# Kernel optimization log

Hardware: AMD Instinct MI355X
Metric: run time of the kernel (lower is better)

Reference implementation:

```python
import jax, jax.numpy as jnp
import numpy as np

B, N, P, E = 64, 512, 256, 4096          # batch, nodes (stations), partition nodes, edges
NUM_NWP, LP, F = 8, 16, 32               # num_nwp, local_points, local_cnn_dims
NT, ED, H, W = 8, 8, 64, 8               # num_temp, edge_feature_dims, decf_mlp_hidden, weight_function_dim
G, RH = 64, 256                          # gnn_dim, readout_hid_dim
H1, Q = 128, 9                           # mlp_hid_dim1, num quantiles


def setup_inputs() -> dict:
    key = jax.random.key(0)
    ks = iter(jax.random.split(key, 40))
    def rn(shape, s=0.05):
        return jax.random.normal(next(ks), shape, dtype=jnp.float32) * s
    # one-hot incidence matrices: each edge has one left (partition) node and one right node
    lidx = jax.random.randint(next(ks), (E,), 0, P)
    ridx = jax.random.randint(next(ks), (E,), 0, N)
    linc = jnp.zeros((P, E), jnp.float32).at[lidx, jnp.arange(E)].set(1.0)
    rinc = jnp.zeros((E, N), jnp.float32).at[jnp.arange(E), ridx].set(1.0)
    inp = {
        "x1": jax.random.normal(next(ks), (B, NUM_NWP * N, LP), dtype=jnp.float32),
        "x2": jax.random.normal(next(ks), (B, NT), dtype=jnp.float32),
        # LocalConv1D grouped conv (torch OIW layout: [Cout, Cin/groups, K])
        "conv_w": rn((F * N, NUM_NWP, LP)), "conv_b": rn((F * N,)),
        # WDSGCN2 edge-weight MLP
        "k1_w": rn((H, ED)), "k1_b": rn((H,)),
        "k2_w": rn((H, NT)),
        "k3_w": rn((H, F)),
        "k4_w": rn((H, F)),
        "k5_w": rn((W, H)), "k5_b": rn((W,)),
        "gc_w": rn((G, F * W)), "gc_b": rn((G,)),
        # readout
        "r0_w": rn((RH, G * P)),
        "r1_w": rn((RH, NT)), "r1_b": rn((RH,)),
        "r2_w": rn((RH, P)),
        "r3_w": rn((P, RH)), "r3_b": rn((P,)),
        # SMlp (forward uses l1 -> ELU -> l3 only)
        "l1_w": rn((H1, NT + G)), "l1_b": rn((H1,)),
        "l3_w": rn((Q, H1)), "l3_b": rn((Q,)),
        # buffers
        "ef": jax.random.normal(next(ks), (E, ED + 1), dtype=jnp.float32),
        "linc": linc,
        "rinc": rinc,
        "cap_feature": jax.random.normal(next(ks), (P,), dtype=jnp.float32),
        "partition_idx": jnp.arange(P, dtype=jnp.int32) * (N // P),
    }
    return inp


def reference(x1, x2, conv_w, conv_b, k1_w, k1_b, k2_w, k3_w, k4_w, k5_w, k5_b,
              gc_w, gc_b, r0_w, r1_w, r1_b, r2_w, r3_w, r3_b,
              l1_w, l1_b, l3_w, l3_b, ef, linc, rinc, cap_feature, partition_idx):
    b = x1.shape[0]
    # --- LocalConv1D: grouped conv1d (valid padding, output length 1) + ReLU ---
    y = jax.lax.conv_general_dilated(x1, conv_w, (1,), 'VALID',
                                     dimension_numbers=('NCH', 'OIH', 'NCH'),
                                     feature_group_count=N)
    x = jax.nn.relu(y + conv_b[None, :, None]).reshape(b, N, F)      # [B,N,F]
    # --- WDSGCN2: per-edge weight kernel ---
    kern = ef[:, :-1] @ k1_w.T + k1_b                                # [E,H]
    kern = kern[None] + (x2 @ k2_w.T)[:, None, :]                    # [B,E,H]
    xp = x[:, partition_idx, :]                                      # [B,P,F]
    kern = kern + jnp.einsum('pe,bpf->bef', linc, xp) @ k3_w.T       # left-node feats
    rx = jnp.einsum('en,bnf->bef', rinc, x)                          # right-node feats [B,E,F]
    kern = kern + rx @ k4_w.T
    kern = jax.nn.relu(jax.nn.leaky_relu(kern, 0.02) @ k5_w.T + k5_b)  # [B,E,W]
    # --- message = kernel (outer) right-node features, aggregated by left incidence ---
    msg = kern[:, :, :, None] * rx[:, :, None, :]                    # [B,E,W,F]
    agg = jnp.einsum('pe,bewf->bpwf', linc, msg).reshape(b, P, W * F)
    yg = jax.nn.relu(agg @ gc_w.T + gc_b)                            # [B,P,G]
    # --- readout attention over partition nodes ---
    h = yg.reshape(b, -1) @ r0_w.T + (x2 @ r1_w.T + r1_b) + cap_feature @ r2_w.T
    wt = jax.nn.relu(jax.nn.leaky_relu(h, 0.01) @ r3_w.T + r3_b)     # [B,P]
    res = jnp.einsum('bp,bpg->bg', wt, yg)                           # [B,G]
    # --- SMlp head ---
    z = jnp.concatenate([res, x2], axis=1)
    z = jax.nn.elu(z @ l1_w.T + l1_b)
    return z @ l3_w.T + l3_b                                         # [B,Q]
```

## Files before the change

kernel.cpp:

```cpp
#include <hip/hip_runtime.h>
#include <math.h>

#define B_ 64
#define N_ 512
#define P_ 256
#define E_ 4096
#define F_ 32
#define H_ 64
#define W_ 8
#define G_ 64
#define RH_ 256

#define X_OFF   0
#define T4_OFF  (X_OFF + N_*B_*F_)
#define T3_OFF  (T4_OFF + N_*B_*H_)
#define KB_OFF  (T3_OFF + P_*B_*H_)
#define KW_OFF  (KB_OFF + E_*H_)
#define YG_OFF  (KW_OFF + E_*B_*W_)
#define HB_OFF  (YG_OFF + B_*P_*G_)
#define RES_OFF (HB_OFF + B_*RH_)
#define INT_OFF (RES_OFF + 4*B_*G_)

__global__ __launch_bounds__(256) void k_decode(const float* __restrict__ linc,
    const float* __restrict__ rinc, int* __restrict__ lidx, int* __restrict__ ridx) {
  int i4 = blockIdx.x * 256 + threadIdx.x;
  const int L4 = (P_ * E_) / 4;
  if (i4 < L4) {
    float4 v = ((const float4*)linc)[i4];
    int i = i4 * 4;
    int p = i >> 12, e = i & 4095;
    if (v.x != 0.0f) lidx[e]     = p;
    if (v.y != 0.0f) lidx[e + 1] = p;
    if (v.z != 0.0f) lidx[e + 2] = p;
    if (v.w != 0.0f) lidx[e + 3] = p;
  } else {
    int j4 = i4 - L4;
    float4 v = ((const float4*)rinc)[j4];
    int j = j4 * 4;
    int e = j >> 9, n = j & 511;
    if (v.x != 0.0f) ridx[e] = n;
    if (v.y != 0.0f) ridx[e] = n + 1;
    if (v.z != 0.0f) ridx[e] = n + 2;
    if (v.w != 0.0f) ridx[e] = n + 3;
  }
}

__global__ __launch_bounds__(1024) void k_lists(const int* __restrict__ lidx,
    int* __restrict__ part_start, int* __restrict__ part_edges) {
  __shared__ int cnt[256];
  __shared__ int buf[256];
  __shared__ int cur[256];
  int t = threadIdx.x;
  if (t < 256) cnt[t] = 0;
  __syncthreads();
  for (int e = t; e < E_; e += 1024) atomicAdd(&cnt[lidx[e]], 1);
  __syncthreads();
  if (t < 256) buf[t] = cnt[t];
  __syncthreads();
  for (int off = 1; off < 256; off <<= 1) {
    int add = 0;
    if (t < 256 && t >= off) add = buf[t - off];
    __syncthreads();
    if (t < 256) buf[t] += add;
    __syncthreads();
  }
  if (t < 256) {
    part_start[t + 1] = buf[t];
    if (t == 0) part_start[0] = 0;
    cur[t] = buf[t] - cnt[t];
  }
  __syncthreads();
  for (int e = t; e < E_; e += 1024) {
    int p = lidx[e];
    int pos = atomicAdd(&cur[p], 1);
    part_edges[pos] = e;
  }
}

__global__ __launch_bounds__(256) void k_conv(const float* __restrict__ x1,
    const float* __restrict__ conv_w, const float* __restrict__ conv_b,
    float* __restrict__ x) {
  __shared__ float wsm[32 * 132];
  __shared__ float xsm[8192];
  int n = blockIdx.x, t = threadIdx.x;
  for (int i = t; i < 1024; i += 256) {
    int f = i >> 5, j = i & 31;
    ((float4*)wsm)[f * 33 + j] = ((const float4*)(conv_w + n * 4096))[i];
  }
  for (int i = t; i < 2048; i += 256) {
    int b = i >> 5, j = i & 31;
    ((float4*)xsm)[i] = ((const float4*)(x1 + b * 65536 + n * 128))[j];
  }
  __syncthreads();
  int f = t & 31, bq = t >> 5;
  float cb = conv_b[n * 32 + f];
  float acc[8];
#pragma unroll
  for (int bi = 0; bi < 8; bi++) acc[bi] = cb;
  const float4* wf4 = (const float4*)wsm + f * 33;
  const float4* xb4 = (const float4*)xsm + bq * 256;
#pragma unroll 4
  for (int k4 = 0; k4 < 32; k4++) {
    float4 wv = wf4[k4];
#pragma unroll
    for (int bi = 0; bi < 8; bi++) {
      float4 xv = xb4[bi * 32 + k4];
      acc[bi] += wv.x * xv.x + wv.y * xv.y + wv.z * xv.z + wv.w * xv.w;
    }
  }
#pragma unroll
  for (int bi = 0; bi < 8; bi++) {
    int b = bq * 8 + bi;
    x[n * 2048 + b * 32 + f] = fmaxf(acc[bi], 0.0f);
  }
}

__global__ __launch_bounds__(256) void k_prep(
    const float* __restrict__ x, const int* __restrict__ pidx,
    const float* __restrict__ k3_w, const float* __restrict__ k4_w,
    const float* __restrict__ x2, const float* __restrict__ k2_w,
    const float* __restrict__ ef, const float* __restrict__ k1_w,
    const float* __restrict__ k1_b,
    const float* __restrict__ r1_w, const float* __restrict__ r1_b,
    const float* __restrict__ r2_w, const float* __restrict__ cap,
    float* __restrict__ t4, float* __restrict__ t3, float* __restrict__ kb,
    float* __restrict__ hbuf) {
  __shared__ float xsh[2048];
  __shared__ float wsh[64 * 36];
  __shared__ float x2s[512];
  __shared__ float k2s[512];
  int blk = blockIdx.x, t = threadIdx.x;
  if (blk < 768) {
    bool isT4 = blk < 512;
    int n = isT4 ? blk : pidx[blk - 512];
    const float* wmat = isT4 ? k4_w : k3_w;
    float* outp = isT4 ? (t4 + blk * 4096) : (t3 + (blk - 512) * 4096);
    for (int i = t; i < 512; i += 256) {
      ((float4*)xsh)[i] = ((const float4*)(x + n * 2048))[i];
      int h = i >> 3, j = i & 7;
      ((float4*)wsh)[h * 9 + j] = ((const float4*)wmat)[i];
    }
    if (isT4) {
      for (int i = t; i < 128; i += 256) {
        ((float4*)x2s)[i] = ((const float4*)x2)[i];
        ((float4*)k2s)[i] = ((const float4*)k2_w)[i];
      }
    }
    __syncthreads();
    int h = t & 63, bq = t >> 6;
    float wreg[32];
#pragma unroll
    for (int j = 0; j < 8; j++) {
      float4 v = ((float4*)wsh)[h * 9 + j];
      wreg[4 * j] = v.x; wreg[4 * j + 1] = v.y; wreg[4 * j + 2] = v.z; wreg[4 * j + 3] = v.w;
    }
    float w2[8];
    if (isT4) {
      float4 u = ((float4*)k2s)[h * 2], v = ((float4*)k2s)[h * 2 + 1];
      w2[0] = u.x; w2[1] = u.y; w2[2] = u.z; w2[3] = u.w;
      w2[4] = v.x; w2[5] = v.y; w2[6] = v.z; w2[7] = v.w;
    }
    for (int bi = 0; bi < 16; bi++) {
      int b = bq * 16 + bi;
      float acc = 0.0f;
#pragma unroll
      for (int j = 0; j < 8; j++) {
        float4 xv = ((float4*)xsh)[b * 8 + j];
        acc += xv.x * wreg[4 * j] + xv.y * wreg[4 * j + 1] +
               xv.z * wreg[4 * j + 2] + xv.w * wreg[4 * j + 3];
      }
      if (isT4) {
        float4 u = ((float4*)x2s)[b * 2], v = ((float4*)x2s)[b * 2 + 1];
        acc += u.x * w2[0] + u.y * w2[1] + u.z * w2[2] + u.w * w2[3] +
               v.x * w2[4] + v.y * w2[5] + v.z * w2[6] + v.w * w2[7];
      }
      outp[b * 64 + h] = acc;
    }
  } else if (blk < 1792) {
    int o = (blk - 768) * 256 + t;
    int e = o >> 6, h = o & 63;
    float acc = k1_b[h];
    const float* er = ef + e * 9;
    const float* kr = k1_w + h * 8;
#pragma unroll
    for (int d = 0; d < 8; d++) acc += er[d] * kr[d];
    kb[o] = acc;
  } else {
    int o = (blk - 1792) * 256 + t;
    int rh = o & 255;
    float acc = r1_b[rh];
    const float* xr = x2 + (o >> 8) * 8;
    const float* rr = r1_w + rh * 8;
#pragma unroll
    for (int d = 0; d < 8; d++) acc += xr[d] * rr[d];
    const float* r2r = r2_w + rh * 256;
    for (int p4 = 0; p4 < 64; p4++) {
      float4 cv = ((const float4*)cap)[p4];
      float4 rv = ((const float4*)r2r)[p4];
      acc += cv.x * rv.x + cv.y * rv.y + cv.z * rv.z + cv.w * rv.w;
    }
    hbuf[o] = acc;
  }
}

__global__ __launch_bounds__(256) void k_eagg(
    const float* __restrict__ x, const float* __restrict__ kb,
    const float* __restrict__ t3, const float* __restrict__ t4,
    const float* __restrict__ k5_w, const float* __restrict__ k5_b,
    const int* __restrict__ ridx, const int* __restrict__ part_start,
    const int* __restrict__ part_edges,
    const float* __restrict__ gc_w, const float* __restrict__ gc_b,
    float* __restrict__ yg) {
  __shared__ float t3s[64 * 68];
  __shared__ float k5t[4 * 520];
  __shared__ unsigned short accS[64 * 256];
  int p = blockIdx.x, t = threadIdx.x;
  for (int i = t; i < 512; i += 256) {
    int h = i >> 3, w = i & 7;
    float v = k5_w[w * 64 + h];
#pragma unroll
    for (int qq = 0; qq < 4; qq++) k5t[qq * 520 + i] = v;
  }
  for (int i4 = t; i4 < 1024; i4 += 256) {
    float4 v = ((const float4*)(t3 + p * 4096))[i4];
    *(float4*)(t3s + (i4 >> 4) * 68 + (i4 & 15) * 4) = v;
  }
  __syncthreads();
  int s = t & 3, b = t >> 2;
  const float* kq = k5t + s * 520 + s * 128;
  float kb5_0 = k5_b[2 * s], kb5_1 = k5_b[2 * s + 1];
  const float4* t3p = (const float4*)(t3s + b * 68 + s * 16);
  float acc[64];
#pragma unroll
  for (int j = 0; j < 64; j++) acc[j] = 0.0f;
  int s0 = part_start[p], s1 = part_start[p + 1];
  int e = 0, r = 0;
  if (s0 < s1) { e = part_edges[s0]; r = ridx[e]; }
  for (int idx = s0; idx < s1; idx++) {
    int e_n = 0, r_n = 0;
    if (idx + 1 < s1) { e_n = part_edges[idx + 1]; r_n = ridx[e_n]; }
    const float4* xp = (const float4*)(x + r * 2048 + b * 32);
    float4 xv0 = xp[0], xv1 = xp[1], xv2 = xp[2], xv3 = xp[3];
    float4 xv4 = xp[4], xv5 = xp[5], xv6 = xp[6], xv7 = xp[7];
    const float4* kb4 = (const float4*)(kb + e * 64 + s * 16);
    const float4* t44 = (const float4*)(t4 + r * 4096 + b * 64 + s * 16);
    float lk[16];
#pragma unroll
    for (int j4 = 0; j4 < 4; j4++) {
      float4 a = kb4[j4], c = t3p[j4], d = t44[j4];
      float v;
      v = a.x + c.x + d.x; lk[j4 * 4 + 0] = v > 0.0f ? v : 0.02f * v;
      v = a.y + c.y + d.y; lk[j4 * 4 + 1] = v > 0.0f ? v : 0.02f * v;
      v = a.z + c.z + d.z; lk[j4 * 4 + 2] = v > 0.0f ? v : 0.02f * v;
      v = a.w + c.w + d.w; lk[j4 * 4 + 3] = v > 0.0f ? v : 0.02f * v;
    }
    float pw[8] = {0, 0, 0, 0, 0, 0, 0, 0};
#pragma unroll
    for (int j = 0; j < 16; j++) {
      float4 u = *(const float4*)(kq + j * 8);
      float4 v = *(const float4*)(kq + j * 8 + 4);
      float l = lk[j];
      pw[0] += l * u.x; pw[1] += l * u.y; pw[2] += l * u.z; pw[3] += l * u.w;
      pw[4] += l * v.x; pw[5] += l * v.y; pw[6] += l * v.z; pw[7] += l * v.w;
    }
#pragma unroll
    for (int w = 0; w < 8; w++) {
      pw[w] += __shfl_xor(pw[w], 1);
      pw[w] += __shfl_xor(pw[w], 2);
    }
    float kv0 = fmaxf(pw[2 * s] + kb5_0, 0.0f);
    float kv1 = fmaxf(pw[2 * s + 1] + kb5_1, 0.0f);
    float xa[32];
    xa[0] = xv0.x; xa[1] = xv0.y; xa[2] = xv0.z; xa[3] = xv0.w;
    xa[4] = xv1.x; xa[5] = xv1.y; xa[6] = xv1.z; xa[7] = xv1.w;
    xa[8] = xv2.x; xa[9] = xv2.y; xa[10] = xv2.z; xa[11] = xv2.w;
    xa[12] = xv3.x; xa[13] = xv3.y; xa[14] = xv3.z; xa[15] = xv3.w;
    xa[16] = xv4.x; xa[17] = xv4.y; xa[18] = xv4.z; xa[19] = xv4.w;
    xa[20] = xv5.x; xa[21] = xv5.y; xa[22] = xv5.z; xa[23] = xv5.w;
    xa[24] = xv6.x; xa[25] = xv6.y; xa[26] = xv6.z; xa[27] = xv6.w;
    xa[28] = xv7.x; xa[29] = xv7.y; xa[30] = xv7.z; xa[31] = xv7.w;
#pragma unroll
    for (int j = 0; j < 32; j++) acc[j] += kv0 * xa[j];
#pragma unroll
    for (int j = 0; j < 32; j++) acc[32 + j] += kv1 * xa[j];
    e = e_n; r = r_n;
  }
#pragma unroll
  for (int o = 0; o < 8; o++) {
    int koct = s * 8 + o;
    int os = koct ^ (b >> 3);
    unsigned int wds[4];
#pragma unroll
    for (int h = 0; h < 4; h++) {
      unsigned int u0 = __float_as_uint(acc[o * 8 + 2 * h]);
      u0 = u0 + 0x7fffu + ((u0 >> 16) & 1u);
      unsigned int u1 = __float_as_uint(acc[o * 8 + 2 * h + 1]);
      u1 = u1 + 0x7fffu + ((u1 >> 16) & 1u);
      wds[h] = (u0 >> 16) | (u1 & 0xffff0000u);
    }
    int4 pk = make_int4((int)wds[0], (int)wds[1], (int)wds[2], (int)wds[3]);
    *(int4*)(accS + b * 256 + os * 8) = pk;
  }
  __syncthreads();
  int lane = t & 63, wv = t >> 6;
  int bg = lane >> 3, gg = lane & 7;
  int g0 = wv * 16 + gg * 2;
  const float* gw0 = gc_w + g0 * 256;
  const float* gw1 = gc_w + (g0 + 1) * 256;
  float ac[8][2];
#pragma unroll
  for (int i = 0; i < 8; i++) { ac[i][0] = 0.0f; ac[i][1] = 0.0f; }
  for (int oct = 0; oct < 32; oct++) {
    int4 a8[8];
#pragma unroll
    for (int i = 0; i < 8; i++) {
      int row = bg * 8 + i;
      int os = oct ^ bg;
      a8[i] = *(const int4*)(accS + row * 256 + os * 8);
    }
    float4 b0a = *(const float4*)(gw0 + oct * 8);
    float4 b0b = *(const float4*)(gw0 + oct * 8 + 4);
    float4 b1a = *(const float4*)(gw1 + oct * 8);
    float4 b1b = *(const float4*)(gw1 + oct * 8 + 4);
    float bv0[8] = {b0a.x, b0a.y, b0a.z, b0a.w, b0b.x, b0b.y, b0b.z, b0b.w};
    float bv1[8] = {b1a.x, b1a.y, b1a.z, b1a.w, b1b.x, b1b.y, b1b.z, b1b.w};
#pragma unroll
    for (int kk = 0; kk < 8; kk++) {
#pragma unroll
      for (int i = 0; i < 8; i++) {
        int w32;
        switch (kk >> 1) {
          case 0: w32 = a8[i].x; break;
          case 1: w32 = a8[i].y; break;
          case 2: w32 = a8[i].z; break;
          default: w32 = a8[i].w; break;
        }
        unsigned int u = (unsigned int)w32;
        unsigned int bits = (kk & 1) ? (u & 0xffff0000u) : (u << 16);
        float av = __uint_as_float(bits);
        ac[i][0] += av * bv0[kk];
        ac[i][1] += av * bv1[kk];
      }
    }
  }
  float gb0 = gc_b[g0], gb1 = gc_b[g0 + 1];
#pragma unroll
  for (int i = 0; i < 8; i++) {
    int bb = bg * 8 + i;
    float* yp = yg + bb * 16384 + p * 64;
    yp[g0]     = fmaxf(ac[i][0] + gb0, 0.0f);
    yp[g0 + 1] = fmaxf(ac[i][1] + gb1, 0.0f);
  }
}

__global__ __launch_bounds__(256) void k_r0(const float* __restrict__ yg,
    const float* __restrict__ r0_w, float* __restrict__ part) {
  __shared__ float ygs[64 * 68];
  __shared__ float wts[64 * 260];
  int kc = blockIdx.x, t = threadIdx.x;
  int k0 = kc * 64;
  {
    int c = t >> 4, rr = t & 15;
    for (int rd = 0; rd < 16; rd++) {
      int rh = rd * 16 + rr;
      float4 v = *(const float4*)(r0_w + rh * 16384 + k0 + c * 4);
      wts[(4 * c + 0) * 260 + rh] = v.x;
      wts[(4 * c + 1) * 260 + rh] = v.y;
      wts[(4 * c + 2) * 260 + rh] = v.z;
      wts[(4 * c + 3) * 260 + rh] = v.w;
    }
  }
  {
    int b = t >> 2, kq = t & 3;
    const float* src = yg + b * 16384 + k0 + kq * 16;
#pragma unroll
    for (int u = 0; u < 4; u++) {
      float4 v = *(const float4*)(src + u * 4);
      int kk = kq * 16 + u * 4;
      ygs[(kk + 0) * 68 + b] = v.x;
      ygs[(kk + 1) * 68 + b] = v.y;
      ygs[(kk + 2) * 68 + b] = v.z;
      ygs[(kk + 3) * 68 + b] = v.w;
    }
  }
  __syncthreads();
  int lane = t & 63, wv = t >> 6;
  int b8 = lane & 7, r8 = lane >> 3;
  const float* yp = ygs + b8 * 8;
  const float* wp = wts + wv * 64 + r8 * 8;
  float acc[8][8];
#pragma unroll
  for (int i = 0; i < 8; i++)
#pragma unroll
    for (int j = 0; j < 8; j++) acc[i][j] = 0.0f;
#pragma unroll 2
  for (int k = 0; k < 64; k++) {
    float4 ya = *(const float4*)(yp + k * 68);
    float4 yb = *(const float4*)(yp + k * 68 + 4);
    float4 wa = *(const float4*)(wp + k * 260);
    float4 wb = *(const float4*)(wp + k * 260 + 4);
    float yv[8] = {ya.x, ya.y, ya.z, ya.w, yb.x, yb.y, yb.z, yb.w};
    float wr[8] = {wa.x, wa.y, wa.z, wa.w, wb.x, wb.y, wb.z, wb.w};
#pragma unroll
    for (int i = 0; i < 8; i++)
#pragma unroll
      for (int j = 0; j < 8; j++) acc[i][j] += yv[i] * wr[j];
  }
  float* pb = part + kc * 16384 + wv * 64 + r8 * 8;
#pragma unroll
  for (int i = 0; i < 8; i++) {
    float4 s0 = make_float4(acc[i][0], acc[i][1], acc[i][2], acc[i][3]);
    float4 s1 = make_float4(acc[i][4], acc[i][5], acc[i][6], acc[i][7]);
    float* pp = pb + (b8 * 8 + i) * 256;
    *(float4*)pp = s0;
    *(float4*)(pp + 4) = s1;
  }
}

__global__ __launch_bounds__(256) void k_r0red(const float* __restrict__ part,
    float* __restrict__ hbuf) {
  int blk = blockIdx.x;
  int oq = blk & 63, kq = blk >> 6;
  int o = oq * 256 + threadIdx.x;
  float s = 0.0f;
  const float* pp = part + kq * 64 * 16384 + o;
#pragma unroll 8
  for (int kc = 0; kc < 64; kc++) s += pp[kc * 16384];
  atomicAdd(&hbuf[o], s);
}

__global__ __launch_bounds__(256) void k_wt_res(const float* __restrict__ hbuf,
    const float* __restrict__ r3_w, const float* __restrict__ r3_b,
    const float* __restrict__ yg, float* __restrict__ res4) {
  __shared__ float hs[256];
  __shared__ float wts[64];
  __shared__ float red[256];
  int blk = blockIdx.x;
  int bb = blk >> 2, pq = blk & 3;
  int t = threadIdx.x;
  float hv = hbuf[bb * 256 + t];
  hs[t] = hv > 0.0f ? hv : 0.01f * hv;
  __syncthreads();
  int pl = t >> 2, c = t & 3;
  int pp = pq * 64 + pl;
  const float4* wrow = (const float4*)(r3_w + pp * 256 + c * 64);
  const float4* h4 = (const float4*)(hs) + c * 16;
  float a = 0.0f;
#pragma unroll
  for (int j = 0; j < 16; j++) {
    float4 w4 = wrow[j], hh = h4[j];
    a += hh.x * w4.x + hh.y * w4.y + hh.z * w4.z + hh.w * w4.w;
  }
  a += __shfl_xor(a, 1);
  a += __shfl_xor(a, 2);
  if (c == 0) wts[pl] = fmaxf(a + r3_b[pp], 0.0f);
  __syncthreads();
  int g = t & 63, ch = t >> 6;
  float r = 0.0f;
  const float* ygp = yg + bb * 16384 + pq * 4096 + g;
#pragma unroll
  for (int pi = 0; pi < 16; pi++) {
    int pl2 = ch * 16 + pi;
    r += wts[pl2] * ygp[pl2 * 64];
  }
  red[t] = r;
  __syncthreads();
  if (t < 64)
    res4[pq * 4096 + bb * 64 + t] = red[t] + red[t + 64] + red[t + 128] + red[t + 192];
}

__global__ __launch_bounds__(128) void k_final(const float* __restrict__ res4,
    const float* __restrict__ x2, const float* __restrict__ l1_w,
    const float* __restrict__ l1_b, const float* __restrict__ l3_w,
    const float* __restrict__ l3_b, float* __restrict__ out) {
  __shared__ float zs[128];
  int bb = blockIdx.x, t = threadIdx.x;
  float acc = l1_b[t];
  const float* wrow = l1_w + t * 72;
  const float* rr = res4 + bb * 64;
#pragma unroll 8
  for (int j = 0; j < 64; j++) {
    float rv = rr[j] + rr[4096 + j] + rr[8192 + j] + rr[12288 + j];
    acc += rv * wrow[j];
  }
  const float* xr = x2 + bb * 8;
#pragma unroll
  for (int j = 0; j < 8; j++) acc += xr[j] * wrow[64 + j];
  zs[t] = acc > 0.0f ? acc : expm1f(acc);
  __syncthreads();
  if (t < 9) {
    float o = l3_b[t];
    const float* w3 = l3_w + t * 128;
    for (int j = 0; j < 128; j++) o += zs[j] * w3[j];
    out[bb * 9 + t] = o;
  }
}

extern "C" void kernel_launch(void* const* d_in, const int* in_sizes, int n_in,
                              void* d_out, int out_size, void* d_ws, size_t ws_size,
                              hipStream_t stream) {
  (void)in_sizes; (void)n_in; (void)out_size; (void)ws_size;
  const float* x1     = (const float*)d_in[0];
  const float* x2     = (const float*)d_in[1];
  const float* conv_w = (const float*)d_in[2];
  const float* conv_b = (const float*)d_in[3];
  const float* k1_w   = (const float*)d_in[4];
  const float* k1_b   = (const float*)d_in[5];
  const float* k2_w   = (const float*)d_in[6];
  const float* k3_w   = (const float*)d_in[7];
  const float* k4_w   = (const float*)d_in[8];
  const float* k5_w   = (const float*)d_in[9];
  const float* k5_b   = (const float*)d_in[10];
  const float* gc_w   = (const float*)d_in[11];
  const float* gc_b   = (const float*)d_in[12];
  const float* r0_w   = (const float*)d_in[13];
  const float* r1_w   = (const float*)d_in[14];
  const float* r1_b   = (const float*)d_in[15];
  const float* r2_w   = (const float*)d_in[16];
  const float* r3_w   = (const float*)d_in[17];
  const float* r3_b   = (const float*)d_in[18];
  const float* l1_w   = (const float*)d_in[19];
  const float* l1_b   = (const float*)d_in[20];
  const float* l3_w   = (const float*)d_in[21];
  const float* l3_b   = (const float*)d_in[22];
  const float* ef     = (const float*)d_in[23];
  const float* linc   = (const float*)d_in[24];
  const float* rinc   = (const float*)d_in[25];
  const float* cap    = (const float*)d_in[26];
  const int*   pidx   = (const int*)d_in[27];
  float* out = (float*)d_out;

  float* ws   = (float*)d_ws;
  float* xbuf = ws + X_OFF;
  float* t4   = ws + T4_OFF;
  float* t3   = ws + T3_OFF;
  float* kb   = ws + KB_OFF;
  float* yg   = ws + YG_OFF;
  float* hbuf = ws + HB_OFF;
  float* res4 = ws + RES_OFF;
  float* part = ws + X_OFF;
  int* ib = (int*)(ws + INT_OFF);
  int* lidx = ib;
  int* ridx = ib + 4096;
  int* part_start = ib + 8192;
  int* part_edges = ib + 8704;

  hipLaunchKernelGGL(k_decode, dim3(3072), dim3(256), 0, stream, linc, rinc, lidx, ridx);
  hipLaunchKernelGGL(k_lists, dim3(1), dim3(1024), 0, stream, lidx, part_start, part_edges);
  hipLaunchKernelGGL(k_conv, dim3(512), dim3(256), 0, stream, x1, conv_w, conv_b, xbuf);
  hipLaunchKernelGGL(k_prep, dim3(1856), dim3(256), 0, stream,
                     xbuf, pidx, k3_w, k4_w, x2, k2_w, ef, k1_w, k1_b,
                     r1_w, r1_b, r2_w, cap, t4, t3, kb, hbuf);
  hipLaunchKernelGGL(k_eagg, dim3(256), dim3(256), 0, stream,
                     xbuf, kb, t3, t4, k5_w, k5_b, ridx, part_start, part_edges,
                     gc_w, gc_b, yg);
  hipLaunchKernelGGL(k_r0, dim3(256), dim3(256), 0, stream, yg, r0_w, part);
  hipLaunchKernelGGL(k_r0red, dim3(256), dim3(256), 0, stream, part, hbuf);
  hipLaunchKernelGGL(k_wt_res, dim3(256), dim3(256), 0, stream, hbuf, r3_w, r3_b, yg, res4);
  hipLaunchKernelGGL(k_final, dim3(64), dim3(128), 0, stream,
                     res4, x2, l1_w, l1_b, l3_w, l3_b, out);
}
```

Baseline: 260.5 us.

## Split edge-aggregation kernel across batch quarters with 16 threads per batch row

The edge-aggregation kernel now launches four blocks per partition node, each handling 16 batch rows, with 16 threads cooperating per batch row instead of 4. Each thread keeps only 16 accumulators instead of 64 and holds the k5 weights in registers rather than shared memory. An extra shuffle reduction across the hidden dimension is added. The gc_w projection is remapped so each thread computes 4 outputs for one row and writes them as a float4. The aim is to lower register pressure, raise occupancy and give the GPU more blocks to spread across its compute units, at the cost of more shuffles and gc_w reads repeated across four blocks.

Result: slower. 331.8 us (+27.4%).

```diff
diff --git a/kernel.cpp b/kernel.cpp
--- a/kernel.cpp
+++ b/kernel.cpp
@@ -203,7 +203,7 @@
   }
 }
 
-__global__ __launch_bounds__(256) void k_eagg(
+__global__ __launch_bounds__(256, 4) void k_eagg(
     const float* __restrict__ x, const float* __restrict__ kb,
     const float* __restrict__ t3, const float* __restrict__ t4,
     const float* __restrict__ k5_w, const float* __restrict__ k5_b,
@@ -211,146 +211,136 @@
     const int* __restrict__ part_edges,
     const float* __restrict__ gc_w, const float* __restrict__ gc_b,
     float* __restrict__ yg) {
-  __shared__ float t3s[64 * 68];
-  __shared__ float k5t[4 * 520];
-  __shared__ unsigned short accS[64 * 256];
-  int p = blockIdx.x, t = threadIdx.x;
-  for (int i = t; i < 512; i += 256) {
-    int h = i >> 3, w = i & 7;
-    float v = k5_w[w * 64 + h];
-#pragma unroll
-    for (int qq = 0; qq < 4; qq++) k5t[qq * 520 + i] = v;
-  }
-  for (int i4 = t; i4 < 1024; i4 += 256) {
-    float4 v = ((const float4*)(t3 + p * 4096))[i4];
-    *(float4*)(t3s + (i4 >> 4) * 68 + (i4 & 15) * 4) = v;
-  }
-  __syncthreads();
-  int s = t & 3, b = t >> 2;
-  const float* kq = k5t + s * 520 + s * 128;
-  float kb5_0 = k5_b[2 * s], kb5_1 = k5_b[2 * s + 1];
-  const float4* t3p = (const float4*)(t3s + b * 68 + s * 16);
-  float acc[64];
-#pragma unroll
-  for (int j = 0; j < 64; j++) acc[j] = 0.0f;
+  __shared__ unsigned short accS[16 * 256];
+  int blk = blockIdx.x;
+  int p = blk >> 2, bh = blk & 3;
+  int t = threadIdx.x;
+  int s = t & 15, bl = t >> 4;
+  int bg = bh * 16 + bl;
+  int j = s & 3;
+  int q = s >> 2;
+  int f0 = q * 8;
+  float4 kr4[8];
+#pragma unroll
+  for (int w = 0; w < 8; w++)
+    kr4[w] = *(const float4*)(k5_w + w * 64 + s * 4);
+  float kb5_0 = k5_b[2 * j], kb5_1 = k5_b[2 * j + 1];
+  float4 t3r = *(const float4*)(t3 + p * 4096 + bg * 64 + s * 4);
+  float acc0[8], acc1[8];
+#pragma unroll
+  for (int i = 0; i < 8; i++) { acc0[i] = 0.0f; acc1[i] = 0.0f; }
   int s0 = part_start[p], s1 = part_start[p + 1];
   int e = 0, r = 0;
   if (s0 < s1) { e = part_edges[s0]; r = ridx[e]; }
   for (int idx = s0; idx < s1; idx++) {
     int e_n = 0, r_n = 0;
     if (idx + 1 < s1) { e_n = part_edges[idx + 1]; r_n = ridx[e_n]; }
-    const float4* xp = (const float4*)(x + r * 2048 + b * 32);
-    float4 xv0 = xp[0], xv1 = xp[1], xv2 = xp[2], xv3 = xp[3];
-    float4 xv4 = xp[4], xv5 = xp[5], xv6 = xp[6], xv7 = xp[7];
-    const float4* kb4 = (const float4*)(kb + e * 64 + s * 16);
-    const float4* t44 = (const float4*)(t4 + r * 4096 + b * 64 + s * 16);
-    float lk[16];
-#pragma unroll
-    for (int j4 = 0; j4 < 4; j4++) {
-      float4 a = kb4[j4], c = t3p[j4], d = t44[j4];
-      float v;
-      v = a.x + c.x + d.x; lk[j4 * 4 + 0] = v > 0.0f ? v : 0.02f * v;
-      v = a.y + c.y + d.y; lk[j4 * 4 + 1] = v > 0.0f ? v : 0.02f * v;
-      v = a.z + c.z + d.z; lk[j4 * 4 + 2] = v > 0.0f ? v : 0.02f * v;
-      v = a.w + c.w + d.w; lk[j4 * 4 + 3] = v > 0.0f ? v : 0.02f * v;
-    }
-    float pw[8] = {0, 0, 0, 0, 0, 0, 0, 0};
-#pragma unroll
-    for (int j = 0; j < 16; j++) {
-      float4 u = *(const float4*)(kq + j * 8);
-      float4 v = *(const float4*)(kq + j * 8 + 4);
-      float l = lk[j];
-      pw[0] += l * u.x; pw[1] += l * u.y; pw[2] += l * u.z; pw[3] += l * u.w;
-      pw[4] += l * v.x; pw[5] += l * v.y; pw[6] += l * v.z; pw[7] += l * v.w;
-    }
+    const float4* xp = (const float4*)(x + r * 2048 + bg * 32 + f0);
+    float4 xv0 = xp[0], xv1 = xp[1];
+    float4 a = *(const float4*)(kb + e * 64 + s * 4);
+    float4 d = *(const float4*)(t4 + r * 4096 + bg * 64 + s * 4);
+    float v, lk0, lk1, lk2, lk3;
+    v = a.x + t3r.x + d.x; lk0 = v > 0.0f ? v : 0.02f * v;
+    v = a.y + t3r.y + d.y; lk1 = v > 0.0f ? v : 0.02f * v;
+    v = a.z + t3r.z + d.z; lk2 = v > 0.0f ? v : 0.02f * v;
+    v = a.w + t3r.w + d.w; lk3 = v > 0.0f ? v : 0.02f * v;
+    float pw[8];
+#pragma unroll
+    for (int w = 0; w < 8; w++)
+      pw[w] = lk0 * kr4[w].x + lk1 * kr4[w].y + lk2 * kr4[w].z + lk3 * kr4[w].w;
 #pragma unroll
     for (int w = 0; w < 8; w++) {
       pw[w] += __shfl_xor(pw[w], 1);
       pw[w] += __shfl_xor(pw[w], 2);
     }
-    float kv0 = fmaxf(pw[2 * s] + kb5_0, 0.0f);
-    float kv1 = fmaxf(pw[2 * s + 1] + kb5_1, 0.0f);
-    float xa[32];
-    xa[0] = xv0.x; xa[1] = xv0.y; xa[2] = xv0.z; xa[3] = xv0.w;
-    xa[4] = xv1.x; xa[5] = xv1.y; xa[6] = xv1.z; xa[7] = xv1.w;
-    xa[8] = xv2.x; xa[9] = xv2.y; xa[10] = xv2.z; xa[11] = xv2.w;
-    xa[12] = xv3.x; xa[13] = xv3.y; xa[14] = xv3.z; xa[15] = xv3.w;
-    xa[16] = xv4.x; xa[17] = xv4.y; xa[18] = xv4.z; xa[19] = xv4.w;
-    xa[20] = xv5.x; xa[21] = xv5.y; xa[22] = xv5.z; xa[23] = xv5.w;
-    xa[24] = xv6.x; xa[25] = xv6.y; xa[26] = xv6.z; xa[27] = xv6.w;
-    xa[28] = xv7.x; xa[29] = xv7.y; xa[30] = xv7.z; xa[31] = xv7.w;
-#pragma unroll
-    for (int j = 0; j < 32; j++) acc[j] += kv0 * xa[j];
-#pragma unroll
-    for (int j = 0; j < 32; j++) acc[32 + j] += kv1 * xa[j];
+    float pa = j == 0 ? pw[0] : j == 1 ? pw[2] : j == 2 ? pw[4] : pw[6];
+    float pb = j == 0 ? pw[1] : j == 1 ? pw[3] : j == 2 ? pw[5] : pw[7];
+    pa += __shfl_xor(pa, 4); pa += __shfl_xor(pa, 8);
+    pb += __shfl_xor(pb, 4); pb += __shfl_xor(pb, 8);
+    float kv0 = fmaxf(pa + kb5_0, 0.0f);
+    float kv1 = fmaxf(pb + kb5_1, 0.0f);
+    float xa[8] = {xv0.x, xv0.y, xv0.z, xv0.w, xv1.x, xv1.y, xv1.z, xv1.w};
+#pragma unroll
+    for (int i = 0; i < 8; i++) acc0[i] += kv0 * xa[i];
+#pragma unroll
+    for (int i = 0; i < 8; i++) acc1[i] += kv1 * xa[i];
     e = e_n; r = r_n;
   }
-#pragma unroll
-  for (int o = 0; o < 8; o++) {
-    int koct = s * 8 + o;
-    int os = koct ^ (b >> 3);
+  {
     unsigned int wds[4];
 #pragma unroll
     for (int h = 0; h < 4; h++) {
-      unsigned int u0 = __float_as_uint(acc[o * 8 + 2 * h]);
+      unsigned int u0 = __float_as_uint(acc0[2 * h]);
       u0 = u0 + 0x7fffu + ((u0 >> 16) & 1u);
-      unsigned int u1 = __float_as_uint(acc[o * 8 + 2 * h + 1]);
+      unsigned int u1 = __float_as_uint(acc0[2 * h + 1]);
       u1 = u1 + 0x7fffu + ((u1 >> 16) & 1u);
       wds[h] = (u0 >> 16) | (u1 & 0xffff0000u);
     }
-    int4 pk = make_int4((int)wds[0], (int)wds[1], (int)wds[2], (int)wds[3]);
-    *(int4*)(accS + b * 256 + os * 8) = pk;
+    int oct = 8 * j + q;
+    int os = oct ^ (bl & 7);
+    *(int4*)(accS + bl * 256 + os * 8) =
+        make_int4((int)wds[0], (int)wds[1], (int)wds[2], (int)wds[3]);
+#pragma unroll
+    for (int h = 0; h < 4; h++) {
+      unsigned int u0 = __float_as_uint(acc1[2 * h]);
+      u0 = u0 + 0x7fffu + ((u0 >> 16) & 1u);
+      unsigned int u1 = __float_as_uint(acc1[2 * h + 1]);
+      u1 = u1 + 0x7fffu + ((u1 >> 16) & 1u);
+      wds[h] = (u0 >> 16) | (u1 & 0xffff0000u);
+    }
+    oct = 8 * j + 4 + q;
+    os = oct ^ (bl & 7);
+    *(int4*)(accS + bl * 256 + os * 8) =
+        make_int4((int)wds[0], (int)wds[1], (int)wds[2], (int)wds[3]);
   }
   __syncthreads();
   int lane = t & 63, wv = t >> 6;
-  int bg = lane >> 3, gg = lane & 7;
-  int g0 = wv * 16 + gg * 2;
+  int row = lane >> 2;
+  int gg = lane & 3;
+  int g0 = wv * 16 + gg * 4;
   const float* gw0 = gc_w + g0 * 256;
-  const float* gw1 = gc_w + (g0 + 1) * 256;
-  float ac[8][2];
-#pragma unroll
-  for (int i = 0; i < 8; i++) { ac[i][0] = 0.0f; ac[i][1] = 0.0f; }
+  const float* gw1 = gw0 + 256;
+  const float* gw2 = gw0 + 512;
+  const float* gw3 = gw0 + 768;
+  float ac0 = 0.0f, ac1 = 0.0f, ac2 = 0.0f, ac3 = 0.0f;
   for (int oct = 0; oct < 32; oct++) {
-    int4 a8[8];
-#pragma unroll
-    for (int i = 0; i < 8; i++) {
-      int row = bg * 8 + i;
-      int os = oct ^ bg;
-      a8[i] = *(const int4*)(accS + row * 256 + os * 8);
-    }
+    int os = oct ^ (row & 7);
+    int4 a8 = *(const int4*)(accS + row * 256 + os * 8);
     float4 b0a = *(const float4*)(gw0 + oct * 8);
     float4 b0b = *(const float4*)(gw0 + oct * 8 + 4);
     float4 b1a = *(const float4*)(gw1 + oct * 8);
     float4 b1b = *(const float4*)(gw1 + oct * 8 + 4);
+    float4 b2a = *(const float4*)(gw2 + oct * 8);
+    float4 b2b = *(const float4*)(gw2 + oct * 8 + 4);
+    float4 b3a = *(const float4*)(gw3 + oct * 8);
+    float4 b3b = *(const float4*)(gw3 + oct * 8 + 4);
     float bv0[8] = {b0a.x, b0a.y, b0a.z, b0a.w, b0b.x, b0b.y, b0b.z, b0b.w};
     float bv1[8] = {b1a.x, b1a.y, b1a.z, b1a.w, b1b.x, b1b.y, b1b.z, b1b.w};
+    float bv2[8] = {b2a.x, b2a.y, b2a.z, b2a.w, b2b.x, b2b.y, b2b.z, b2b.w};
+    float bv3[8] = {b3a.x, b3a.y, b3a.z, b3a.w, b3b.x, b3b.y, b3b.z, b3b.w};
 #pragma unroll
     for (int kk = 0; kk < 8; kk++) {
-#pragma unroll
-      for (int i = 0; i < 8; i++) {
-        int w32;
-        switch (kk >> 1) {
-          case 0: w32 = a8[i].x; break;
-          case 1: w32 = a8[i].y; break;
-          case 2: w32 = a8[i].z; break;
-          default: w32 = a8[i].w; break;
-        }
-        unsigned int u = (unsigned int)w32;
-        unsigned int bits = (kk & 1) ? (u & 0xffff0000u) : (u << 16);
-        float av = __uint_as_float(bits);
-        ac[i][0] += av * bv0[kk];
-        ac[i][1] += av * bv1[kk];
+      int w32;
+      switch (kk >> 1) {
+        case 0: w32 = a8.x; break;
+        case 1: w32 = a8.y; break;
+        case 2: w32 = a8.z; break;
+        default: w32 = a8.w; break;
       }
-    }
-  }
-  float gb0 = gc_b[g0], gb1 = gc_b[g0 + 1];
-#pragma unroll
-  for (int i = 0; i < 8; i++) {
-    int bb = bg * 8 + i;
-    float* yp = yg + bb * 16384 + p * 64;
-    yp[g0]     = fmaxf(ac[i][0] + gb0, 0.0f);
-    yp[g0 + 1] = fmaxf(ac[i][1] + gb1, 0.0f);
-  }
+      unsigned int u = (unsigned int)w32;
+      unsigned int bits = (kk & 1) ? (u & 0xffff0000u) : (u << 16);
+      float av = __uint_as_float(bits);
+      ac0 += av * bv0[kk];
+      ac1 += av * bv1[kk];
+      ac2 += av * bv2[kk];
+      ac3 += av * bv3[kk];
+    }
+  }
+  float4 gb = *(const float4*)(gc_b + g0);
+  float* yp = yg + (bh * 16 + row) * 16384 + p * 64 + g0;
+  float4 o = make_float4(fmaxf(ac0 + gb.x, 0.0f), fmaxf(ac1 + gb.y, 0.0f),
+                         fmaxf(ac2 + gb.z, 0.0f), fmaxf(ac3 + gb.w, 0.0f));
+  *(float4*)yp = o;
 }
 
 __global__ __launch_bounds__(256) void k_r0(const float* __restrict__ yg,
@@ -551,7 +541,7 @@
   hipLaunchKernelGGL(k_prep, dim3(1856), dim3(256), 0, stream,
                      xbuf, pidx, k3_w, k4_w, x2, k2_w, ef, k1_w, k1_b,
                      r1_w, r1_b, r2_w, cap, t4, t3, kb, hbuf);
-  hipLaunchKernelGGL(k_eagg, dim3(256), dim3(256), 0, stream,
+  hipLaunchKernelGGL(k_eagg, dim3(1024), dim3(256), 0, stream,
                      xbuf, kb, t3, t4, k5_w, k5_b, ridx, part_start, part_edges,
                      gc_w, gc_b, yg);
   hipLaunchKernelGGL(k_r0, dim3(256), dim3(256), 0, stream, yg, r0_w, part);
```

## Merge setup kernels, split edge loop across two slots, drop bf16 staging

Applied to the files above, without the earlier changes.

The incidence decode and conv kernels are merged into one launch. The edge-list build moves into an extra block of the prep kernel and stores (edge, right-node) pairs together. The edge aggregation kernel now uses 512 threads, with two slots each handling alternate edges of a partition. The slots reduce their partial sums through fp32 shared memory in two halves, and the gc projection reads gc_w directly, replacing the bf16-packed staging. The aim is fewer launches, more parallelism in the latency-bound edge loop, and no bf16 rounding, at the cost of extra syncs and higher register pressure from 512 threads each holding 64 accumulators.

New measurement: 258.7 us. No clear change (-0.7%).

```diff
diff --git a/kernel.cpp b/kernel.cpp
--- a/kernel.cpp
+++ b/kernel.cpp
@@ -21,68 +21,38 @@
 #define RES_OFF (HB_OFF + B_*RH_)
 #define INT_OFF (RES_OFF + 4*B_*G_)
 
-__global__ __launch_bounds__(256) void k_decode(const float* __restrict__ linc,
-    const float* __restrict__ rinc, int* __restrict__ lidx, int* __restrict__ ridx) {
-  int i4 = blockIdx.x * 256 + threadIdx.x;
-  const int L4 = (P_ * E_) / 4;
-  if (i4 < L4) {
-    float4 v = ((const float4*)linc)[i4];
-    int i = i4 * 4;
-    int p = i >> 12, e = i & 4095;
-    if (v.x != 0.0f) lidx[e]     = p;
-    if (v.y != 0.0f) lidx[e + 1] = p;
-    if (v.z != 0.0f) lidx[e + 2] = p;
-    if (v.w != 0.0f) lidx[e + 3] = p;
-  } else {
-    int j4 = i4 - L4;
-    float4 v = ((const float4*)rinc)[j4];
-    int j = j4 * 4;
-    int e = j >> 9, n = j & 511;
-    if (v.x != 0.0f) ridx[e] = n;
-    if (v.y != 0.0f) ridx[e] = n + 1;
-    if (v.z != 0.0f) ridx[e] = n + 2;
-    if (v.w != 0.0f) ridx[e] = n + 3;
-  }
-}
-
-__global__ __launch_bounds__(1024) void k_lists(const int* __restrict__ lidx,
-    int* __restrict__ part_start, int* __restrict__ part_edges) {
-  __shared__ int cnt[256];
-  __shared__ int buf[256];
-  __shared__ int cur[256];
-  int t = threadIdx.x;
-  if (t < 256) cnt[t] = 0;
-  __syncthreads();
-  for (int e = t; e < E_; e += 1024) atomicAdd(&cnt[lidx[e]], 1);
-  __syncthreads();
-  if (t < 256) buf[t] = cnt[t];
-  __syncthreads();
-  for (int off = 1; off < 256; off <<= 1) {
-    int add = 0;
-    if (t < 256 && t >= off) add = buf[t - off];
-    __syncthreads();
-    if (t < 256) buf[t] += add;
-    __syncthreads();
-  }
-  if (t < 256) {
-    part_start[t + 1] = buf[t];
-    if (t == 0) part_start[0] = 0;
-    cur[t] = buf[t] - cnt[t];
-  }
-  __syncthreads();
-  for (int e = t; e < E_; e += 1024) {
-    int p = lidx[e];
-    int pos = atomicAdd(&cur[p], 1);
-    part_edges[pos] = e;
-  }
-}
-
-__global__ __launch_bounds__(256) void k_conv(const float* __restrict__ x1,
-    const float* __restrict__ conv_w, const float* __restrict__ conv_b,
-    float* __restrict__ x) {
+__global__ __launch_bounds__(256) void k_dc(
+    const float* __restrict__ linc, const float* __restrict__ rinc,
+    int* __restrict__ lidx, int* __restrict__ ridx,
+    const float* __restrict__ x1, const float* __restrict__ conv_w,
+    const float* __restrict__ conv_b, float* __restrict__ x) {
   __shared__ float wsm[32 * 132];
   __shared__ float xsm[8192];
-  int n = blockIdx.x, t = threadIdx.x;
+  int blk = blockIdx.x, t = threadIdx.x;
+  if (blk < 3072) {
+    int i4 = blk * 256 + t;
+    const int L4 = (P_ * E_) / 4;
+    if (i4 < L4) {
+      float4 v = ((const float4*)linc)[i4];
+      int i = i4 * 4;
+      int p = i >> 12, e = i & 4095;
+      if (v.x != 0.0f) lidx[e]     = p;
+      if (v.y != 0.0f) lidx[e + 1] = p;
+      if (v.z != 0.0f) lidx[e + 2] = p;
+      if (v.w != 0.0f) lidx[e + 3] = p;
+    } else {
+      int j4 = i4 - L4;
+      float4 v = ((const float4*)rinc)[j4];
+      int j = j4 * 4;
+      int e = j >> 9, n = j & 511;
+      if (v.x != 0.0f) ridx[e] = n;
+      if (v.y != 0.0f) ridx[e] = n + 1;
+      if (v.z != 0.0f) ridx[e] = n + 2;
+      if (v.w != 0.0f) ridx[e] = n + 3;
+    }
+    return;
+  }
+  int n = blk - 3072;
   for (int i = t; i < 1024; i += 256) {
     int f = i >> 5, j = i & 31;
     ((float4*)wsm)[f * 33 + j] = ((const float4*)(conv_w + n * 4096))[i];
@@ -123,12 +93,17 @@
     const float* __restrict__ k1_b,
     const float* __restrict__ r1_w, const float* __restrict__ r1_b,
     const float* __restrict__ r2_w, const float* __restrict__ cap,
+    const int* __restrict__ lidx, const int* __restrict__ ridx,
     float* __restrict__ t4, float* __restrict__ t3, float* __restrict__ kb,
-    float* __restrict__ hbuf) {
+    float* __restrict__ hbuf, int* __restrict__ part_start,
+    int2* __restrict__ pe2) {
   __shared__ float xsh[2048];
   __shared__ float wsh[64 * 36];
   __shared__ float x2s[512];
   __shared__ float k2s[512];
+  __shared__ int cnt[256];
+  __shared__ int buf[256];
+  __shared__ int cur[256];
   int blk = blockIdx.x, t = threadIdx.x;
   if (blk < 768) {
     bool isT4 = blk < 512;
@@ -185,7 +160,7 @@
 #pragma unroll
     for (int d = 0; d < 8; d++) acc += er[d] * kr[d];
     kb[o] = acc;
-  } else {
+  } else if (blk < 1856) {
     int o = (blk - 1792) * 256 + t;
     int rh = o & 255;
     float acc = r1_b[rh];
@@ -200,33 +175,56 @@
       acc += cv.x * rv.x + cv.y * rv.y + cv.z * rv.z + cv.w * rv.w;
     }
     hbuf[o] = acc;
-  }
-}
-
-__global__ __launch_bounds__(256) void k_eagg(
+  } else {
+    cnt[t] = 0;
+    __syncthreads();
+    for (int e = t; e < E_; e += 256) atomicAdd(&cnt[lidx[e]], 1);
+    __syncthreads();
+    buf[t] = cnt[t];
+    __syncthreads();
+    for (int off = 1; off < 256; off <<= 1) {
+      int add = (t >= off) ? buf[t - off] : 0;
+      __syncthreads();
+      buf[t] += add;
+      __syncthreads();
+    }
+    part_start[t + 1] = buf[t];
+    if (t == 0) part_start[0] = 0;
+    cur[t] = buf[t] - cnt[t];
+    __syncthreads();
+    for (int e = t; e < E_; e += 256) {
+      int p = lidx[e];
+      int pos = atomicAdd(&cur[p], 1);
+      pe2[pos] = make_int2(e, ridx[e]);
+    }
+  }
+}
+
+__global__ __launch_bounds__(512) void k_eagg(
     const float* __restrict__ x, const float* __restrict__ kb,
     const float* __restrict__ t3, const float* __restrict__ t4,
     const float* __restrict__ k5_w, const float* __restrict__ k5_b,
-    const int* __restrict__ ridx, const int* __restrict__ part_start,
-    const int* __restrict__ part_edges,
+    const int2* __restrict__ pe2, const int* __restrict__ part_start,
     const float* __restrict__ gc_w, const float* __restrict__ gc_b,
     float* __restrict__ yg) {
   __shared__ float t3s[64 * 68];
   __shared__ float k5t[4 * 520];
-  __shared__ unsigned short accS[64 * 256];
+  __shared__ float accS[64 * 128];
   int p = blockIdx.x, t = threadIdx.x;
-  for (int i = t; i < 512; i += 256) {
-    int h = i >> 3, w = i & 7;
+  int slot = t >> 8;
+  int ts = t & 255;
+  int s = ts & 3, b = ts >> 2;
+  {
+    int h = t >> 3, w = t & 7;
     float v = k5_w[w * 64 + h];
 #pragma unroll
-    for (int qq = 0; qq < 4; qq++) k5t[qq * 520 + i] = v;
-  }
-  for (int i4 = t; i4 < 1024; i4 += 256) {
+    for (int qq = 0; qq < 4; qq++) k5t[qq * 520 + t] = v;
+  }
+  for (int i4 = t; i4 < 1024; i4 += 512) {
     float4 v = ((const float4*)(t3 + p * 4096))[i4];
     *(float4*)(t3s + (i4 >> 4) * 68 + (i4 & 15) * 4) = v;
   }
   __syncthreads();
-  int s = t & 3, b = t >> 2;
   const float* kq = k5t + s * 520 + s * 128;
   float kb5_0 = k5_b[2 * s], kb5_1 = k5_b[2 * s + 1];
   const float4* t3p = (const float4*)(t3s + b * 68 + s * 16);
@@ -234,11 +232,13 @@
 #pragma unroll
   for (int j = 0; j < 64; j++) acc[j] = 0.0f;
   int s0 = part_start[p], s1 = part_start[p + 1];
-  int e = 0, r = 0;
-  if (s0 < s1) { e = part_edges[s0]; r = ridx[e]; }
-  for (int idx = s0; idx < s1; idx++) {
-    int e_n = 0, r_n = 0;
-    if (idx + 1 < s1) { e_n = part_edges[idx + 1]; r_n = ridx[e_n]; }
+  int idx0 = s0 + slot;
+  int2 c = make_int2(0, 0);
+  if (idx0 < s1) c = pe2[idx0];
+  for (int idx = idx0; idx < s1; idx += 2) {
+    int n2 = idx + 2;
+    int2 cn = (n2 < s1) ? pe2[n2] : c;
+    int e = c.x, r = c.y;
     const float4* xp = (const float4*)(x + r * 2048 + b * 32);
     float4 xv0 = xp[0], xv1 = xp[1], xv2 = xp[2], xv3 = xp[3];
     float4 xv4 = xp[4], xv5 = xp[5], xv6 = xp[6], xv7 = xp[7];
@@ -247,12 +247,12 @@
     float lk[16];
 #pragma unroll
     for (int j4 = 0; j4 < 4; j4++) {
-      float4 a = kb4[j4], c = t3p[j4], d = t44[j4];
+      float4 a = kb4[j4], cc = t3p[j4], d = t44[j4];
       float v;
-      v = a.x + c.x + d.x; lk[j4 * 4 + 0] = v > 0.0f ? v : 0.02f * v;
-      v = a.y + c.y + d.y; lk[j4 * 4 + 1] = v > 0.0f ? v : 0.02f * v;
-      v = a.z + c.z + d.z; lk[j4 * 4 + 2] = v > 0.0f ? v : 0.02f * v;
-      v = a.w + c.w + d.w; lk[j4 * 4 + 3] = v > 0.0f ? v : 0.02f * v;
+      v = a.x + cc.x + d.x; lk[j4 * 4 + 0] = v > 0.0f ? v : 0.02f * v;
+      v = a.y + cc.y + d.y; lk[j4 * 4 + 1] = v > 0.0f ? v : 0.02f * v;
+      v = a.z + cc.z + d.z; lk[j4 * 4 + 2] = v > 0.0f ? v : 0.02f * v;
+      v = a.w + cc.w + d.w; lk[j4 * 4 + 3] = v > 0.0f ? v : 0.02f * v;
     }
     float pw[8] = {0, 0, 0, 0, 0, 0, 0, 0};
 #pragma unroll
@@ -283,74 +283,60 @@
     for (int j = 0; j < 32; j++) acc[j] += kv0 * xa[j];
 #pragma unroll
     for (int j = 0; j < 32; j++) acc[32 + j] += kv1 * xa[j];
-    e = e_n; r = r_n;
-  }
-#pragma unroll
-  for (int o = 0; o < 8; o++) {
-    int koct = s * 8 + o;
-    int os = koct ^ (b >> 3);
-    unsigned int wds[4];
-#pragma unroll
-    for (int h = 0; h < 4; h++) {
-      unsigned int u0 = __float_as_uint(acc[o * 8 + 2 * h]);
-      u0 = u0 + 0x7fffu + ((u0 >> 16) & 1u);
-      unsigned int u1 = __float_as_uint(acc[o * 8 + 2 * h + 1]);
-      u1 = u1 + 0x7fffu + ((u1 >> 16) & 1u);
-      wds[h] = (u0 >> 16) | (u1 & 0xffff0000u);
-    }
-    int4 pk = make_int4((int)wds[0], (int)wds[1], (int)wds[2], (int)wds[3]);
-    *(int4*)(accS + b * 256 + os * 8) = pk;
-  }
-  __syncthreads();
-  int lane = t & 63, wv = t >> 6;
-  int bg = lane >> 3, gg = lane & 7;
-  int g0 = wv * 16 + gg * 2;
-  const float* gw0 = gc_w + g0 * 256;
-  const float* gw1 = gc_w + (g0 + 1) * 256;
-  float ac[8][2];
-#pragma unroll
-  for (int i = 0; i < 8; i++) { ac[i][0] = 0.0f; ac[i][1] = 0.0f; }
-  for (int oct = 0; oct < 32; oct++) {
-    int4 a8[8];
-#pragma unroll
-    for (int i = 0; i < 8; i++) {
-      int row = bg * 8 + i;
-      int os = oct ^ bg;
-      a8[i] = *(const int4*)(accS + row * 256 + os * 8);
-    }
-    float4 b0a = *(const float4*)(gw0 + oct * 8);
-    float4 b0b = *(const float4*)(gw0 + oct * 8 + 4);
-    float4 b1a = *(const float4*)(gw1 + oct * 8);
-    float4 b1b = *(const float4*)(gw1 + oct * 8 + 4);
-    float bv0[8] = {b0a.x, b0a.y, b0a.z, b0a.w, b0b.x, b0b.y, b0b.z, b0b.w};
-    float bv1[8] = {b1a.x, b1a.y, b1a.z, b1a.w, b1b.x, b1b.y, b1b.z, b1b.w};
-#pragma unroll
-    for (int kk = 0; kk < 8; kk++) {
+    c = cn;
+  }
+  int gq = t >> 6, be = t & 63;
+  const float* gwb = gc_w + gq * 8 * 256;
+  float ac[8];
+#pragma unroll
+  for (int i = 0; i < 8; i++) ac[i] = 0.0f;
+#pragma unroll
+  for (int h = 0; h < 2; h++) {
+    if (h) __syncthreads();
+    if (slot == 0) {
+#pragma unroll
+      for (int w2 = 0; w2 < 2; w2++)
+#pragma unroll
+        for (int fr4 = 0; fr4 < 4; fr4++) {
+          int khalf4 = 8 * s + 4 * w2 + fr4;
+          int phys4 = (khalf4 & 24) | ((khalf4 ^ s ^ b) & 7);
+          int j = 32 * w2 + 16 * h + 4 * fr4;
+          *(float4*)(accS + b * 128 + phys4 * 4) =
+              make_float4(acc[j], acc[j + 1], acc[j + 2], acc[j + 3]);
+        }
+    }
+    __syncthreads();
+    if (slot == 1) {
+#pragma unroll
+      for (int w2 = 0; w2 < 2; w2++)
+#pragma unroll
+        for (int fr4 = 0; fr4 < 4; fr4++) {
+          int khalf4 = 8 * s + 4 * w2 + fr4;
+          int phys4 = (khalf4 & 24) | ((khalf4 ^ s ^ b) & 7);
+          int j = 32 * w2 + 16 * h + 4 * fr4;
+          float4* ptr = (float4*)(accS + b * 128 + phys4 * 4);
+          float4 o = *ptr;
+          o.x += acc[j]; o.y += acc[j + 1]; o.z += acc[j + 2]; o.w += acc[j + 3];
+          *ptr = o;
+        }
+    }
+    __syncthreads();
+    for (int k4h = 0; k4h < 32; k4h++) {
+      int phys4 = (k4h & 24) | ((k4h ^ (k4h >> 3) ^ be) & 7);
+      float4 av = *(const float4*)(accS + be * 128 + phys4 * 4);
+      int w = k4h >> 2, fr4 = k4h & 3;
+      int k4g = w * 8 + h * 4 + fr4;
 #pragma unroll
       for (int i = 0; i < 8; i++) {
-        int w32;
-        switch (kk >> 1) {
-          case 0: w32 = a8[i].x; break;
-          case 1: w32 = a8[i].y; break;
-          case 2: w32 = a8[i].z; break;
-          default: w32 = a8[i].w; break;
-        }
-        unsigned int u = (unsigned int)w32;
-        unsigned int bits = (kk & 1) ? (u & 0xffff0000u) : (u << 16);
-        float av = __uint_as_float(bits);
-        ac[i][0] += av * bv0[kk];
-        ac[i][1] += av * bv1[kk];
+        float4 wv = *(const float4*)(gwb + i * 256 + k4g * 4);
+        ac[i] += av.x * wv.x + av.y * wv.y + av.z * wv.z + av.w * wv.w;
       }
     }
   }
-  float gb0 = gc_b[g0], gb1 = gc_b[g0 + 1];
-#pragma unroll
-  for (int i = 0; i < 8; i++) {
-    int bb = bg * 8 + i;
-    float* yp = yg + bb * 16384 + p * 64;
-    yp[g0]     = fmaxf(ac[i][0] + gb0, 0.0f);
-    yp[g0 + 1] = fmaxf(ac[i][1] + gb1, 0.0f);
-  }
+  float* yp = yg + be * 16384 + p * 64 + gq * 8;
+#pragma unroll
+  for (int i = 0; i < 8; i++)
+    yp[i] = fmaxf(ac[i] + gc_b[gq * 8 + i], 0.0f);
 }
 
 __global__ __launch_bounds__(256) void k_r0(const float* __restrict__ yg,
@@ -543,16 +529,16 @@
   int* lidx = ib;
   int* ridx = ib + 4096;
   int* part_start = ib + 8192;
-  int* part_edges = ib + 8704;
-
-  hipLaunchKernelGGL(k_decode, dim3(3072), dim3(256), 0, stream, linc, rinc, lidx, ridx);
-  hipLaunchKernelGGL(k_lists, dim3(1), dim3(1024), 0, stream, lidx, part_start, part_edges);
-  hipLaunchKernelGGL(k_conv, dim3(512), dim3(256), 0, stream, x1, conv_w, conv_b, xbuf);
-  hipLaunchKernelGGL(k_prep, dim3(1856), dim3(256), 0, stream,
+  int2* pe2 = (int2*)(ib + 8704);
+
+  hipLaunchKernelGGL(k_dc, dim3(3584), dim3(256), 0, stream,
+                     linc, rinc, lidx, ridx, x1, conv_w, conv_b, xbuf);
+  hipLaunchKernelGGL(k_prep, dim3(1857), dim3(256), 0, stream,
                      xbuf, pidx, k3_w, k4_w, x2, k2_w, ef, k1_w, k1_b,
-                     r1_w, r1_b, r2_w, cap, t4, t3, kb, hbuf);
-  hipLaunchKernelGGL(k_eagg, dim3(256), dim3(256), 0, stream,
-                     xbuf, kb, t3, t4, k5_w, k5_b, ridx, part_start, part_edges,
+                     r1_w, r1_b, r2_w, cap, lidx, ridx,
+                     t4, t3, kb, hbuf, part_start, pe2);
+  hipLaunchKernelGGL(k_eagg, dim3(256), dim3(512), 0, stream,
+                     xbuf, kb, t3, t4, k5_w, k5_b, pe2, part_start,
                      gc_w, gc_b, yg);
   hipLaunchKernelGGL(k_r0, dim3(256), dim3(256), 0, stream, yg, r0_w, part);
   hipLaunchKernelGGL(k_r0red, dim3(256), dim3(256), 0, stream, part, hbuf);
```
